# Kernel tuning notes

Measured on AMD Instinct MI355X. Metric: run time of the kernel, lower is better.

Reference implementation:

```python
import jax, jax.numpy as jnp
import numpy as np


def setup_inputs() -> dict:
    key = jax.random.key(0)
    k1, k2 = jax.random.split(key)
    x = jax.random.normal(k1, (2048, 64), dtype=jnp.float32)
    y = jax.random.normal(k2, (2048, 64), dtype=jnp.float32)
    return {"x": x, "y": y}


def reference(x, y):
    # Faithful to torch module: broadcast diff -> square -> sum over last dim -> sqrt.
    # diff: [N, M, D]
    diff = x[..., :, None, :] - y[..., None, :, :]
    sum_sq_diff = jnp.sum(diff * diff, axis=-1)  # [N, M]
    return jnp.sqrt(sum_sq_diff)
```

## Files before the change

### kernel.cpp

```cpp
#include <hip/hip_runtime.h>
#include <hip/hip_bf16.h>
#include <math.h>

#define DD 64

typedef __bf16 bf16x8 __attribute__((ext_vector_type(8)));
typedef float f32x4 __attribute__((ext_vector_type(4)));

__device__ inline bf16x8 cvt8n(const float4 a, const float4 b, float& s) {
  bf16x8 r;
  float t;
  r[0] = (__bf16)a.x; t = (float)r[0]; s = fmaf(t, t, s);
  r[1] = (__bf16)a.y; t = (float)r[1]; s = fmaf(t, t, s);
  r[2] = (__bf16)a.z; t = (float)r[2]; s = fmaf(t, t, s);
  r[3] = (__bf16)a.w; t = (float)r[3]; s = fmaf(t, t, s);
  r[4] = (__bf16)b.x; t = (float)r[4]; s = fmaf(t, t, s);
  r[5] = (__bf16)b.y; t = (float)r[5]; s = fmaf(t, t, s);
  r[6] = (__bf16)b.z; t = (float)r[6]; s = fmaf(t, t, s);
  r[7] = (__bf16)b.w; t = (float)r[7]; s = fmaf(t, t, s);
  return r;
}

__global__ __launch_bounds__(256) void cdist_fused(
    const float* __restrict__ x, const float* __restrict__ y,
    float* __restrict__ out, int N, int M) {
  const int bid = blockIdx.x;
  const int swz = (bid & 7) * 128 + (bid >> 3);
  const int bx = swz & 31;
  const int by = swz >> 5;

  const int lane = threadIdx.x & 63;
  const int wid  = threadIdx.x >> 6;
  const int wr = wid >> 1, wc = wid & 1;
  const int i0 = by * 64 + wr * 32;
  const int j0 = bx * 64 + wc * 32;
  const int lrow = lane & 15;
  const int kgrp = lane >> 4;

  __shared__ float sny[4][32];

  bf16x8 a[2][2], b[2][2];
  float sa[2] = {0.f, 0.f}, sb[2] = {0.f, 0.f};
  #pragma unroll
  for (int m = 0; m < 2; ++m) {
    #pragma unroll
    for (int ks = 0; ks < 2; ++ks) {
      const float* px = &x[(size_t)(i0 + m * 16 + lrow) * DD + ks * 32 + kgrp * 8];
      a[m][ks] = cvt8n(*reinterpret_cast<const float4*>(px),
                       *reinterpret_cast<const float4*>(px + 4), sa[m]);
      const float* py = &y[(size_t)(j0 + m * 16 + lrow) * DD + ks * 32 + kgrp * 8];
      b[m][ks] = cvt8n(*reinterpret_cast<const float4*>(py),
                       *reinterpret_cast<const float4*>(py + 4), sb[m]);
    }
  }

  #pragma unroll
  for (int m = 0; m < 2; ++m) {
    sa[m] += __shfl_xor(sa[m], 16, 64);
    sa[m] += __shfl_xor(sa[m], 32, 64);
    sb[m] += __shfl_xor(sb[m], 16, 64);
    sb[m] += __shfl_xor(sb[m], 32, 64);
  }

  if (kgrp == 0) {
    sny[wid][lrow]      = sb[0];
    sny[wid][16 + lrow] = sb[1];
  }

  f32x4 acc[2][2] = {};
  #pragma unroll
  for (int ks = 0; ks < 2; ++ks)
    #pragma unroll
    for (int n = 0; n < 2; ++n)
      #pragma unroll
      for (int m = 0; m < 2; ++m)
        acc[n][m] = __builtin_amdgcn_mfma_f32_16x16x32_bf16(
            b[n][ks], a[m][ks], acc[n][m], 0, 0, 0);

  #pragma unroll
  for (int n = 0; n < 2; ++n) {
    const float4 nyv = *reinterpret_cast<const float4*>(&sny[wid][n * 16 + kgrp * 4]);
    #pragma unroll
    for (int m = 0; m < 2; ++m) {
      f32x4 res;
      float d2;
      d2 = fmaf(-2.0f, acc[n][m][0], sa[m] + nyv.x);
      res[0] = __builtin_amdgcn_sqrtf(fmaxf(d2, 0.f));
      d2 = fmaf(-2.0f, acc[n][m][1], sa[m] + nyv.y);
      res[1] = __builtin_amdgcn_sqrtf(fmaxf(d2, 0.f));
      d2 = fmaf(-2.0f, acc[n][m][2], sa[m] + nyv.z);
      res[2] = __builtin_amdgcn_sqrtf(fmaxf(d2, 0.f));
      d2 = fmaf(-2.0f, acc[n][m][3], sa[m] + nyv.w);
      res[3] = __builtin_amdgcn_sqrtf(fmaxf(d2, 0.f));
      __builtin_nontemporal_store(
          res, reinterpret_cast<f32x4*>(
              &out[(size_t)(i0 + m * 16 + lrow) * M + j0 + n * 16 + kgrp * 4]));
    }
  }
}

extern "C" void kernel_launch(void* const* d_in, const int* in_sizes, int n_in,
                              void* d_out, int out_size, void* d_ws, size_t ws_size,
                              hipStream_t stream) {
  const float* x = (const float*)d_in[0];
  const float* y = (const float*)d_in[1];
  float* out = (float*)d_out;
  const int N = in_sizes[0] / DD;
  const int M = in_sizes[1] / DD;

  const int nblocks = (N / 64) * (M / 64);
  cdist_fused<<<dim3(nblocks), dim3(256), 0, stream>>>(x, y, out, N, M);
}
```

Measured before the change: 15.07 us.

## Process two column tiles per block, reusing the converted x fragments

Each block now covers a 64x128 output tile instead of 64x64, halving the grid to 512 blocks. The x rows are loaded and converted to bf16 once and reused for two column sub-tiles, and the y loads for both sub-tiles are issued up front. This cuts redundant x loads, conversions and block launch overhead, in exchange for more registers per thread and fewer blocks to spread across the CUs.

```diff
diff --git a/kernel.cpp b/kernel.cpp
--- a/kernel.cpp
+++ b/kernel.cpp
@@ -25,32 +25,42 @@
     const float* __restrict__ x, const float* __restrict__ y,
     float* __restrict__ out, int N, int M) {
   const int bid = blockIdx.x;
-  const int swz = (bid & 7) * 128 + (bid >> 3);
-  const int bx = swz & 31;
-  const int by = swz >> 5;
+  const int swz = (bid & 7) * 64 + (bid >> 3);
+  const int bxp = swz & 15;
+  const int by  = swz >> 4;
 
   const int lane = threadIdx.x & 63;
   const int wid  = threadIdx.x >> 6;
   const int wr = wid >> 1, wc = wid & 1;
-  const int i0 = by * 64 + wr * 32;
-  const int j0 = bx * 64 + wc * 32;
+  const int i0  = by * 64 + wr * 32;
+  const int j00 = bxp * 128 + wc * 32;
   const int lrow = lane & 15;
   const int kgrp = lane >> 4;
 
-  __shared__ float sny[4][32];
+  __shared__ float sny[4][2][32];
 
-  bf16x8 a[2][2], b[2][2];
-  float sa[2] = {0.f, 0.f}, sb[2] = {0.f, 0.f};
+  bf16x8 a[2][2];
+  float sa[2] = {0.f, 0.f};
   #pragma unroll
   for (int m = 0; m < 2; ++m) {
+    const float* px = &x[(size_t)(i0 + m * 16 + lrow) * DD + kgrp * 8];
+    a[m][0] = cvt8n(*reinterpret_cast<const float4*>(px),
+                    *reinterpret_cast<const float4*>(px + 4), sa[m]);
+    a[m][1] = cvt8n(*reinterpret_cast<const float4*>(px + 32),
+                    *reinterpret_cast<const float4*>(px + 36), sa[m]);
+  }
+
+  float4 yv[2][2][2][2];
+  #pragma unroll
+  for (int it = 0; it < 2; ++it) {
     #pragma unroll
-    for (int ks = 0; ks < 2; ++ks) {
-      const float* px = &x[(size_t)(i0 + m * 16 + lrow) * DD + ks * 32 + kgrp * 8];
-      a[m][ks] = cvt8n(*reinterpret_cast<const float4*>(px),
-                       *reinterpret_cast<const float4*>(px + 4), sa[m]);
-      const float* py = &y[(size_t)(j0 + m * 16 + lrow) * DD + ks * 32 + kgrp * 8];
-      b[m][ks] = cvt8n(*reinterpret_cast<const float4*>(py),
-                       *reinterpret_cast<const float4*>(py + 4), sb[m]);
+    for (int n = 0; n < 2; ++n) {
+      const float* py =
+          &y[(size_t)(j00 + it * 64 + n * 16 + lrow) * DD + kgrp * 8];
+      yv[it][n][0][0] = *reinterpret_cast<const float4*>(py);
+      yv[it][n][0][1] = *reinterpret_cast<const float4*>(py + 4);
+      yv[it][n][1][0] = *reinterpret_cast<const float4*>(py + 32);
+      yv[it][n][1][1] = *reinterpret_cast<const float4*>(py + 36);
     }
   }
 
@@ -58,43 +68,58 @@
   for (int m = 0; m < 2; ++m) {
     sa[m] += __shfl_xor(sa[m], 16, 64);
     sa[m] += __shfl_xor(sa[m], 32, 64);
-    sb[m] += __shfl_xor(sb[m], 16, 64);
-    sb[m] += __shfl_xor(sb[m], 32, 64);
   }
 
-  if (kgrp == 0) {
-    sny[wid][lrow]      = sb[0];
-    sny[wid][16 + lrow] = sb[1];
-  }
+  #pragma unroll
+  for (int it = 0; it < 2; ++it) {
+    bf16x8 b[2][2];
+    float sb[2] = {0.f, 0.f};
+    #pragma unroll
+    for (int n = 0; n < 2; ++n) {
+      b[n][0] = cvt8n(yv[it][n][0][0], yv[it][n][0][1], sb[n]);
+      b[n][1] = cvt8n(yv[it][n][1][0], yv[it][n][1][1], sb[n]);
+    }
+    #pragma unroll
+    for (int n = 0; n < 2; ++n) {
+      sb[n] += __shfl_xor(sb[n], 16, 64);
+      sb[n] += __shfl_xor(sb[n], 32, 64);
+    }
+    if (kgrp == 0) {
+      sny[wid][it][lrow]      = sb[0];
+      sny[wid][it][16 + lrow] = sb[1];
+    }
 
-  f32x4 acc[2][2] = {};
-  #pragma unroll
-  for (int ks = 0; ks < 2; ++ks)
+    f32x4 acc[2][2] = {};
     #pragma unroll
-    for (int n = 0; n < 2; ++n)
+    for (int ks = 0; ks < 2; ++ks)
       #pragma unroll
-      for (int m = 0; m < 2; ++m)
-        acc[n][m] = __builtin_amdgcn_mfma_f32_16x16x32_bf16(
-            b[n][ks], a[m][ks], acc[n][m], 0, 0, 0);
+      for (int n = 0; n < 2; ++n)
+        #pragma unroll
+        for (int m = 0; m < 2; ++m)
+          acc[n][m] = __builtin_amdgcn_mfma_f32_16x16x32_bf16(
+              b[n][ks], a[m][ks], acc[n][m], 0, 0, 0);
 
-  #pragma unroll
-  for (int n = 0; n < 2; ++n) {
-    const float4 nyv = *reinterpret_cast<const float4*>(&sny[wid][n * 16 + kgrp * 4]);
+    const int j0 = j00 + it * 64;
     #pragma unroll
-    for (int m = 0; m < 2; ++m) {
-      f32x4 res;
-      float d2;
-      d2 = fmaf(-2.0f, acc[n][m][0], sa[m] + nyv.x);
-      res[0] = __builtin_amdgcn_sqrtf(fmaxf(d2, 0.f));
-      d2 = fmaf(-2.0f, acc[n][m][1], sa[m] + nyv.y);
-      res[1] = __builtin_amdgcn_sqrtf(fmaxf(d2, 0.f));
-      d2 = fmaf(-2.0f, acc[n][m][2], sa[m] + nyv.z);
-      res[2] = __builtin_amdgcn_sqrtf(fmaxf(d2, 0.f));
-      d2 = fmaf(-2.0f, acc[n][m][3], sa[m] + nyv.w);
-      res[3] = __builtin_amdgcn_sqrtf(fmaxf(d2, 0.f));
-      __builtin_nontemporal_store(
-          res, reinterpret_cast<f32x4*>(
-              &out[(size_t)(i0 + m * 16 + lrow) * M + j0 + n * 16 + kgrp * 4]));
+    for (int n = 0; n < 2; ++n) {
+      const float4 nyv =
+          *reinterpret_cast<const float4*>(&sny[wid][it][n * 16 + kgrp * 4]);
+      #pragma unroll
+      for (int m = 0; m < 2; ++m) {
+        f32x4 res;
+        float d2;
+        d2 = fmaf(-2.0f, acc[n][m][0], sa[m] + nyv.x);
+        res[0] = __builtin_amdgcn_sqrtf(fmaxf(d2, 0.f));
+        d2 = fmaf(-2.0f, acc[n][m][1], sa[m] + nyv.y);
+        res[1] = __builtin_amdgcn_sqrtf(fmaxf(d2, 0.f));
+        d2 = fmaf(-2.0f, acc[n][m][2], sa[m] + nyv.z);
+        res[2] = __builtin_amdgcn_sqrtf(fmaxf(d2, 0.f));
+        d2 = fmaf(-2.0f, acc[n][m][3], sa[m] + nyv.w);
+        res[3] = __builtin_amdgcn_sqrtf(fmaxf(d2, 0.f));
+        __builtin_nontemporal_store(
+            res, reinterpret_cast<f32x4*>(
+                &out[(size_t)(i0 + m * 16 + lrow) * M + j0 + n * 16 + kgrp * 4]));
+      }
     }
   }
 }
@@ -108,6 +133,6 @@
   const int N = in_sizes[0] / DD;
   const int M = in_sizes[1] / DD;
 
-  const int nblocks = (N / 64) * (M / 64);
+  const int nblocks = (N / 64) * (M / 128);
   cdist_fused<<<dim3(nblocks), dim3(256), 0, stream>>>(x, y, out, N, M);
 }
```

Measured after the change: 13.89 us. 7.8% less time.
